# Performance work log

Measured on AMD Instinct MI355X. Metric: run time of the kernel, lower is better.

## Reference

```python
import jax, jax.numpy as jnp
import numpy as np

B, T, D = 2, 2048, 2048
H, G = 16, 4            # query heads, kv groups
HD = D // H             # head_dim = 128
GS = H // G             # group_size = 4
EPS = 1e-6
ROPE_BASE = 10000.0


def setup_inputs() -> dict:
    key = jax.random.key(0)
    ks = jax.random.split(key, 5)
    s = 0.02
    return {
        "x": jax.random.normal(ks[0], (B, T, D), jnp.float32),
        "Wq": jax.random.normal(ks[1], (H * HD, D), jnp.float32) * s,
        "Wk": jax.random.normal(ks[2], (G * HD, D), jnp.float32) * s,
        "Wv": jax.random.normal(ks[3], (G * HD, D), jnp.float32) * s,
        "Wo": jax.random.normal(ks[4], (D, H * HD), jnp.float32) * s,
        "qn_w": jnp.ones((HD,), jnp.float32),
        "kn_w": jnp.ones((HD,), jnp.float32),
    }


def _rmsnorm(x, w):
    var = jnp.mean(x * x, axis=-1, keepdims=True)
    return x * jax.lax.rsqrt(var + EPS) * w


def _rope_tables(t, d):
    inv_freq = 1.0 / (ROPE_BASE ** (jnp.arange(0, d, 2, dtype=jnp.float32) / d))
    freqs = jnp.arange(t, dtype=jnp.float32)[:, None] * inv_freq[None, :]
    emb = jnp.concatenate([freqs, freqs], axis=-1)  # [T, d]
    return jnp.cos(emb), jnp.sin(emb)


def _apply_rope(x, cos, sin):
    # x: [b, h, t, d]
    d2 = x.shape[-1] // 2
    x1, x2 = x[..., :d2], x[..., d2:]
    rot = jnp.concatenate([-x2, x1], axis=-1)
    return x * cos + rot * sin


def reference(x, Wq, Wk, Wv, Wo, qn_w, kn_w):
    b, t, _ = x.shape
    q = (x @ Wq.T).reshape(b, t, H, HD).transpose(0, 2, 1, 3)  # [b,H,t,hd]
    k = (x @ Wk.T).reshape(b, t, G, HD).transpose(0, 2, 1, 3)  # [b,G,t,hd]
    v = (x @ Wv.T).reshape(b, t, G, HD).transpose(0, 2, 1, 3)

    q = _rmsnorm(q, qn_w)
    k = _rmsnorm(k, kn_w)

    cos, sin = _rope_tables(t, HD)
    q = _apply_rope(q, cos, sin)
    k = _apply_rope(k, cos, sin)

    # torch code scales q by hd^-0.5, then SDPA applies default hd^-0.5 again
    scale = (HD ** -0.5) * (HD ** -0.5)

    # GQA without materializing repeat_interleave: group query heads
    qg = q.reshape(b, G, GS, t, HD)
    scores = jnp.einsum("bgxqd,bgkd->bgxqk", qg, k) * scale  # [b,G,GS,t,t]
    causal = jnp.tril(jnp.ones((t, t), bool))
    scores = jnp.where(causal, scores, -jnp.inf)
    attn = jax.nn.softmax(scores, axis=-1)
    ctx = jnp.einsum("bgxqk,bgkd->bgxqd", attn, v)  # [b,G,GS,t,hd]
    ctx = ctx.reshape(b, H, t, HD).transpose(0, 2, 1, 3).reshape(b, t, H * HD)
    return ctx @ Wo.T
```

## Files before the change

kernel.cpp:

```cpp
#include <hip/hip_runtime.h>
#include <hip/hip_bf16.h>

#define B_ 2
#define T_ 2048
#define D_ 2048
#define H_ 16
#define G_ 4
#define HD_ 128
#define GS_ (H_/G_)

typedef _Float16 half8 __attribute__((ext_vector_type(8)));
typedef _Float16 half2_t __attribute__((ext_vector_type(2)));
typedef float f32x4 __attribute__((ext_vector_type(4)));
typedef float f32x16 __attribute__((ext_vector_type(16)));
typedef int int4_t __attribute__((ext_vector_type(4)));

#define KV_TILE_BYTES 35840
#define KROW_F16 136
#define VROW_F16 72
#define VBASE_F16 8704

__global__ void cvt_f16(const float* __restrict__ in, _Float16* __restrict__ out, int n) {
    int i = blockIdx.x * blockDim.x + threadIdx.x;
    int stride = blockDim.x * gridDim.x;
    for (; i < n; i += stride) out[i] = (_Float16)in[i];
}

__global__ void rope_tables_k(float* __restrict__ cosT, float* __restrict__ sinT) {
    int i = blockIdx.x * blockDim.x + threadIdx.x;
    int t = i >> 6, l = i & 63;
    float inv_freq = powf(10000.0f, -((float)(2 * l)) / 128.0f);
    float a = (float)t * inv_freq;
    cosT[i] = cosf(a);
    sinT[i] = sinf(a);
}

__global__ void __launch_bounds__(256) gemm_tile(const _Float16* __restrict__ A,
                                                 const _Float16* __restrict__ B0,
                                                 float* __restrict__ C0, int n0t,
                                                 const _Float16* __restrict__ B1,
                                                 float* __restrict__ C1, int n1t,
                                                 const _Float16* __restrict__ B2,
                                                 float* __restrict__ C2, int n2t,
                                                 int Kd) {
    __shared__ _Float16 sA[128 * 32];
    __shared__ _Float16 sB[128 * 32];

    int tid = threadIdx.x;
    int w = tid >> 6, lane = tid & 63;
    int l15 = lane & 15, g4 = lane >> 4;
    int wm = w >> 1, wn = w & 1;

    int y = blockIdx.y;
    const _Float16* Bsel;
    float* Csel;
    int ldc, cb;
    if (y < n0t)            { Bsel = B0; Csel = C0; ldc = n0t * 128; cb = y; }
    else if (y < n0t + n1t) { Bsel = B1; Csel = C1; ldc = n1t * 128; cb = y - n0t; }
    else                    { Bsel = B2; Csel = C2; ldc = n2t * 128; cb = y - n0t - n1t; }

    const _Float16* Ab = A + (size_t)(blockIdx.x * 128) * Kd;
    const _Float16* Bb = Bsel + (size_t)(cb * 128) * Kd;

    int s0 = w * 128 + lane;
    int s1 = s0 + 64;
    int r0 = s0 >> 2, c0 = s0 & 3;
    int r1 = s1 >> 2, c1 = s1 & 3;
    size_t ga0 = (size_t)r0 * Kd + c0 * 8;
    size_t ga1 = (size_t)r1 * Kd + c1 * 8;
    _Float16* lds_a0 = sA + (size_t)(w * 2) * 512;
    _Float16* lds_a1 = sA + (size_t)(w * 2 + 1) * 512;
    _Float16* lds_b0 = sB + (size_t)(w * 2) * 512;
    _Float16* lds_b1 = sB + (size_t)(w * 2 + 1) * 512;

    #define STAGE(K0)                                                                     \
        do {                                                                              \
            __builtin_amdgcn_global_load_lds(                                             \
                (const __attribute__((address_space(1))) unsigned int*)(Ab + ga0 + (K0)), \
                (__attribute__((address_space(3))) unsigned int*)lds_a0, 16, 0, 0);       \
            __builtin_amdgcn_global_load_lds(                                             \
                (const __attribute__((address_space(1))) unsigned int*)(Ab + ga1 + (K0)), \
                (__attribute__((address_space(3))) unsigned int*)lds_a1, 16, 0, 0);       \
            __builtin_amdgcn_global_load_lds(                                             \
                (const __attribute__((address_space(1))) unsigned int*)(Bb + ga0 + (K0)), \
                (__attribute__((address_space(3))) unsigned int*)lds_b0, 16, 0, 0);       \
            __builtin_amdgcn_global_load_lds(                                             \
                (const __attribute__((address_space(1))) unsigned int*)(Bb + ga1 + (K0)), \
                (__attribute__((address_space(3))) unsigned int*)lds_b1, 16, 0, 0);       \
        } while (0)

    f32x4 acc[4][4];
    #pragma unroll
    for (int i = 0; i < 4; i++)
        #pragma unroll
        for (int j = 0; j < 4; j++) acc[i][j] = (f32x4){0.f, 0.f, 0.f, 0.f};

    STAGE(0);

    int nIt = Kd >> 5;
    for (int it = 0; it < nIt; ++it) {
        __syncthreads();

        half8 af[4], bf[4];
        #pragma unroll
        for (int mi = 0; mi < 4; mi++)
            af[mi] = *(const half8*)&sA[(wm * 64 + mi * 16 + l15) * 32 + g4 * 8];
        #pragma unroll
        for (int ni = 0; ni < 4; ni++)
            bf[ni] = *(const half8*)&sB[(wn * 64 + ni * 16 + l15) * 32 + g4 * 8];

        #pragma unroll
        for (int mi = 0; mi < 4; mi++)
            #pragma unroll
            for (int ni = 0; ni < 4; ni++)
                acc[mi][ni] = __builtin_amdgcn_mfma_f32_16x16x32_f16(af[mi], bf[ni], acc[mi][ni], 0, 0, 0);

        if (it + 1 < nIt) {
            __syncthreads();
            STAGE((size_t)(it + 1) * 32);
        }
    }
    #undef STAGE

    int rbase = blockIdx.x * 128 + wm * 64 + g4 * 4;
    int cbase = cb * 128 + wn * 64 + l15;
    #pragma unroll
    for (int mi = 0; mi < 4; mi++)
        #pragma unroll
        for (int r = 0; r < 4; r++) {
            float* crow = Csel + (size_t)(rbase + mi * 16 + r) * ldc + cbase;
            #pragma unroll
            for (int ni = 0; ni < 4; ni++) crow[ni * 16] = acc[mi][ni][r];
        }
}

__global__ void rmsnorm_rope_k(float* __restrict__ X, const float* __restrict__ w,
                               const float* __restrict__ cosT, const float* __restrict__ sinT,
                               int heads, float outScale, _Float16* __restrict__ outH) {
    int gw = (int)((blockIdx.x * (size_t)blockDim.x + threadIdx.x) >> 6);
    int lane = threadIdx.x & 63;
    float* row = X + (size_t)gw * HD_;
    int t = (gw / heads) % T_;
    float x0 = row[lane];
    float x1 = row[lane + 64];
    float ss = x0 * x0 + x1 * x1;
    #pragma unroll
    for (int off = 1; off < 64; off <<= 1) ss += __shfl_xor(ss, off);
    float inv = rsqrtf(ss * (1.0f / 128.0f) + 1e-6f);
    float n0 = x0 * inv * w[lane];
    float n1 = x1 * inv * w[lane + 64];
    float c = cosT[t * 64 + lane];
    float s = sinT[t * 64 + lane];
    float r0 = (n0 * c - n1 * s) * outScale;
    float r1 = (n1 * c + n0 * s) * outScale;
    if (outH) {
        outH[(size_t)gw * HD_ + lane]      = (_Float16)r0;
        outH[(size_t)gw * HD_ + lane + 64] = (_Float16)r1;
    } else {
        row[lane]      = r0;
        row[lane + 64] = r1;
    }
}

__global__ void __launch_bounds__(256) pack_kv(const float* __restrict__ kf,
                                               const float* __restrict__ vf,
                                               _Float16* __restrict__ img) {
    int bid = blockIdx.x;
    int tile = bid & 31, g = (bid >> 5) & 3, b = bid >> 7;
    int tid = threadIdx.x;
    _Float16* out = img + (size_t)bid * (KV_TILE_BYTES / 2);

    #pragma unroll
    for (int it = 0; it < 5; it++) {
        int gi = tid + 256 * it;
        if (gi < 64 * 17) {
            int key = gi / 17, gr = gi % 17;
            half8 hv = (half8){0, 0, 0, 0, 0, 0, 0, 0};
            if (gr < 16) {
                const float* src = kf + ((size_t)((b * T_ + tile * 64 + key) * G_ + g)) * HD_ + gr * 8;
                #pragma unroll
                for (int j = 0; j < 8; j++) hv[j] = (_Float16)src[j];
            }
            *(half8*)(out + (size_t)gi * 8) = hv;
        }
    }
    #pragma unroll
    for (int it = 0; it < 5; it++) {
        int vi = tid + 256 * it;
        if (vi < 128 * 9) {
            int d = vi / 9, gr = vi % 9;
            half8 hv = (half8){0, 0, 0, 0, 0, 0, 0, 0};
            if (gr < 8) {
                const float* src = vf + ((size_t)((b * T_ + tile * 64 + gr * 8) * G_ + g)) * HD_ + d;
                #pragma unroll
                for (int j = 0; j < 8; j++) hv[j] = (_Float16)src[(size_t)j * (G_ * HD_)];
            }
            *(half8*)(out + VBASE_F16 + (size_t)vi * 8) = hv;
        }
    }
}

__global__ void __launch_bounds__(256, 2) attn_mfma4(const _Float16* __restrict__ qh,
                                                     const _Float16* __restrict__ kvimg,
                                                     _Float16* __restrict__ ctx) {
    int id = blockIdx.x;
    int hlf = id >> 8, rr0 = id & 255;
    int qb = hlf ? (15 - (rr0 & 15)) : (rr0 & 15);
    int hb = (rr0 >> 4) | (hlf << 4);
    int h = hb & 15, b = hb >> 4;
    int g = h >> 2;

    int tid = threadIdx.x;
    int w = tid >> 6, lane = tid & 63;
    int l31 = lane & 31, hi = lane >> 5;

    __shared__ __align__(16) char sKV[2][KV_TILE_BYTES];

    int qW = qb * 128 + w * 32;
    int qme = qW + l31;

    half8 qfrag[8];
    {
        const _Float16* qrow = qh + ((size_t)(b * T_ + qme)) * (H_ * HD_) + h * HD_ + hi * 8;
        #pragma unroll
        for (int ks = 0; ks < 8; ks++) qfrag[ks] = *(const half8*)(qrow + ks * 16);
    }

    f32x16 o[4];
    #pragma unroll
    for (int dt2 = 0; dt2 < 4; dt2++)
        #pragma unroll
        for (int r = 0; r < 16; r++) o[dt2][r] = 0.f;
    float m = -INFINITY, lsum = 0.f;

    const char* ibase = (const char*)kvimg + (size_t)((b * 4 + g) * 32) * KV_TILE_BYTES;

    #define STAGE_T(BUF, KT)                                                                       \
        do {                                                                                       \
            const char* src_ = ibase + (size_t)(KT) * KV_TILE_BYTES;                               \
            char* dst_ = &sKV[BUF][0];                                                             \
            _Pragma("unroll")                                                                      \
            for (int i_ = 0; i_ < 9; i_++) {                                                       \
                int c_ = w + 4 * i_;                                                               \
                if (c_ < 35) {                                                                     \
                    __builtin_amdgcn_global_load_lds(                                              \
                        (const __attribute__((address_space(1))) unsigned int*)(src_ + c_ * 1024 + lane * 16), \
                        (__attribute__((address_space(3))) unsigned int*)(dst_ + c_ * 1024 + lane * 16), 16, 0, 0); \
                }                                                                                  \
            }                                                                                      \
        } while (0)

    int nt = 2 * qb + 2;
    int ktmax_w = (qW + 31) >> 6;

    STAGE_T(0, 0);
    int cur = 0;

    for (int kt = 0; kt < nt; kt++) {
        __syncthreads();
        if (kt + 1 < nt) STAGE_T(cur ^ 1, kt + 1);

        if (kt <= ktmax_w) {
            const char* bufK = &sKV[cur][0];
            const char* bufV = &sKV[cur][0] + VBASE_F16 * 2;

            f32x16 stc[2];
            #pragma unroll
            for (int kt2 = 0; kt2 < 2; kt2++)
                #pragma unroll
                for (int r = 0; r < 16; r++) stc[kt2][r] = 0.f;

            __builtin_amdgcn_s_setprio(1);
            #pragma unroll
            for (int ks = 0; ks < 8; ks++) {
                #pragma unroll
                for (int kt2 = 0; kt2 < 2; kt2++) {
                    half8 kfr = *(const half8*)(bufK + (kt2 * 32 + l31) * (KROW_F16 * 2) + ks * 32 + hi * 16);
                    stc[kt2] = __builtin_amdgcn_mfma_f32_32x32x16_f16(kfr, qfrag[ks], stc[kt2], 0, 0, 0);
                }
            }
            __builtin_amdgcn_s_setprio(0);

            #pragma unroll
            for (int kt2 = 0; kt2 < 2; kt2++)
                #pragma unroll
                for (int reg = 0; reg < 16; reg++) {
                    int key = kt * 64 + kt2 * 32 + 8 * (reg >> 2) + 4 * hi + (reg & 3);
                    float v = stc[kt2][reg];
                    stc[kt2][reg] = (key <= qme) ? v : -INFINITY;
                }

            float pmax = -INFINITY;
            #pragma unroll
            for (int kt2 = 0; kt2 < 2; kt2++)
                #pragma unroll
                for (int reg = 0; reg < 16; reg++) pmax = fmaxf(pmax, stc[kt2][reg]);
            pmax = fmaxf(pmax, __shfl_xor(pmax, 32));

            if (__any(!(pmax - m <= 8.0f))) {
                float nm = fmaxf(m, pmax);
                float alpha = __expf(m - nm);
                lsum *= alpha;
                #pragma unroll
                for (int reg = 0; reg < 16; reg++) {
                    float ar = __shfl(alpha, 8 * (reg >> 2) + 4 * hi + (reg & 3));
                    #pragma unroll
                    for (int dt2 = 0; dt2 < 4; dt2++) o[dt2][reg] *= ar;
                }
                m = nm;
            }

            float rsum = 0.f;
            #pragma unroll
            for (int kt2 = 0; kt2 < 2; kt2++)
                #pragma unroll
                for (int reg = 0; reg < 16; reg++) {
                    float e = __expf(stc[kt2][reg] - m);
                    stc[kt2][reg] = e;
                    rsum += e;
                }
            rsum += __shfl_xor(rsum, 32);
            lsum += rsum;

            int pk[16];
            #pragma unroll
            for (int kt2 = 0; kt2 < 2; kt2++)
                #pragma unroll
                for (int oo = 0; oo < 4; oo++)
                    #pragma unroll
                    for (int c = 0; c < 2; c++) {
                        half2_t hp;
                        hp[0] = (_Float16)stc[kt2][4 * oo + 2 * c];
                        hp[1] = (_Float16)stc[kt2][4 * oo + 2 * c + 1];
                        pk[kt2 * 8 + 2 * oo + c] = __builtin_bit_cast(int, hp);
                    }

            __builtin_amdgcn_s_setprio(1);
            #pragma unroll
            for (int ks = 0; ks < 4; ks++) {
                int base = (ks >> 1) * 8 + (ks & 1) * 4;
                int z0 = hi ? pk[base + 0] : pk[base + 2];
                int z1 = hi ? pk[base + 1] : pk[base + 3];
                int xz0 = __shfl_xor(z0, 32);
                int xz1 = __shfl_xor(z1, 32);
                int4_t pi;
                pi[0] = hi ? xz0 : pk[base + 0];
                pi[1] = hi ? xz1 : pk[base + 1];
                pi[2] = hi ? pk[base + 2] : xz0;
                pi[3] = hi ? pk[base + 3] : xz1;
                half8 pfrag = __builtin_bit_cast(half8, pi);
                #pragma unroll
                for (int dt2 = 0; dt2 < 4; dt2++) {
                    half8 vfr = *(const half8*)(bufV + (dt2 * 32 + l31) * (VROW_F16 * 2) + ks * 32 + hi * 16);
                    o[dt2] = __builtin_amdgcn_mfma_f32_32x32x16_f16(pfrag, vfr, o[dt2], 0, 0, 0);
                }
            }
            __builtin_amdgcn_s_setprio(0);
        }
        cur ^= 1;
    }
    #undef STAGE_T

    float invl = 1.0f / lsum;
    #pragma unroll
    for (int reg = 0; reg < 16; reg++) {
        int qrow = 8 * (reg >> 2) + 4 * hi + (reg & 3);
        float ir = __shfl(invl, qrow);
        _Float16* orow = ctx + (size_t)(b * T_ + qW + qrow) * (H_ * HD_) + h * HD_ + l31;
        #pragma unroll
        for (int dt2 = 0; dt2 < 4; dt2++)
            orow[dt2 * 32] = (_Float16)(o[dt2][reg] * ir);
    }
}

extern "C" void kernel_launch(void* const* d_in, const int* in_sizes, int n_in,
                              void* d_out, int out_size, void* d_ws, size_t ws_size,
                              hipStream_t stream) {
    const float* x   = (const float*)d_in[0];
    const float* Wq  = (const float*)d_in[1];
    const float* Wk  = (const float*)d_in[2];
    const float* Wv  = (const float*)d_in[3];
    const float* Wo  = (const float*)d_in[4];
    const float* qnw = (const float*)d_in[5];
    const float* knw = (const float*)d_in[6];
    float* out = (float*)d_out;

    char* ws = (char*)d_ws;
    size_t off = 0;
    auto alloc = [&](size_t bytes) {
        char* p = ws + off;
        off += (bytes + 255) & ~(size_t)255;
        return p;
    };
    _Float16* x_h  = (_Float16*)alloc((size_t)B_ * T_ * D_ * 2);
    _Float16* wq_h = (_Float16*)alloc((size_t)H_ * HD_ * D_ * 2);
    _Float16* wk_h = (_Float16*)alloc((size_t)G_ * HD_ * D_ * 2);
    _Float16* wv_h = (_Float16*)alloc((size_t)G_ * HD_ * D_ * 2);
    _Float16* wo_h = (_Float16*)alloc((size_t)D_ * H_ * HD_ * 2);
    float* q_f = (float*)alloc((size_t)B_ * T_ * H_ * HD_ * 4);
    float* k_f = (float*)alloc((size_t)B_ * T_ * G_ * HD_ * 4);
    float* v_f = (float*)alloc((size_t)B_ * T_ * G_ * HD_ * 4);
    _Float16* ctx_h = (_Float16*)alloc((size_t)B_ * T_ * H_ * HD_ * 2);
    float* cosT = (float*)alloc((size_t)T_ * 64 * 4);
    float* sinT = (float*)alloc((size_t)T_ * 64 * 4);

    _Float16* q_h   = x_h;
    _Float16* kvimg = wq_h;

    cvt_f16<<<2048, 256, 0, stream>>>(x,  x_h,  B_ * T_ * D_);
    cvt_f16<<<2048, 256, 0, stream>>>(Wq, wq_h, H_ * HD_ * D_);
    cvt_f16<<<1024, 256, 0, stream>>>(Wk, wk_h, G_ * HD_ * D_);
    cvt_f16<<<1024, 256, 0, stream>>>(Wv, wv_h, G_ * HD_ * D_);
    cvt_f16<<<2048, 256, 0, stream>>>(Wo, wo_h, D_ * H_ * HD_);
    rope_tables_k<<<(T_ * 64) / 256, 256, 0, stream>>>(cosT, sinT);

    gemm_tile<<<dim3(32, 24), 256, 0, stream>>>(x_h, wq_h, q_f, 16,
                                                wk_h, k_f, 4,
                                                wv_h, v_f, 4, D_);

    rmsnorm_rope_k<<<(B_ * T_ * H_) / 4, 256, 0, stream>>>(q_f, qnw, cosT, sinT, H_, 1.0f / 128.0f, q_h);
    rmsnorm_rope_k<<<(B_ * T_ * G_) / 4, 256, 0, stream>>>(k_f, knw, cosT, sinT, G_, 1.0f, nullptr);

    pack_kv<<<256, 256, 0, stream>>>(k_f, v_f, kvimg);

    attn_mfma4<<<512, 256, 0, stream>>>(q_h, kvimg, ctx_h);

    gemm_tile<<<dim3(32, 16), 256, 0, stream>>>(ctx_h, wo_h, out, 16,
                                                nullptr, nullptr, 0,
                                                nullptr, nullptr, 0, H_ * HD_);
}
```

Baseline: 248.7 us.

## Fuse conversions and norms, shrink GEMM tiles to 64x128 with block swizzle

Merges the five fp32-to-fp16 conversion launches into one vectorized kernel and merges the Q and K RMSNorm+RoPE launches into one. Switches the projection GEMMs to 64x128 tiles with a 1D grid and an XCD-style block remap, doubling the workgroup count so the CUs fill better. Per-block reuse drops (the B tile is loaded twice as often) in exchange for more parallelism and fewer launches.

```diff
diff --git a/kernel.cpp b/kernel.cpp
--- a/kernel.cpp
+++ b/kernel.cpp
@@ -20,10 +20,35 @@
 #define VROW_F16 72
 #define VBASE_F16 8704
 
-__global__ void cvt_f16(const float* __restrict__ in, _Float16* __restrict__ out, int n) {
-    int i = blockIdx.x * blockDim.x + threadIdx.x;
+#define C0_ 1048576
+#define C1_ 1572864
+#define C2_ 1703936
+#define C3_ 1835008
+#define C4_ 2359296
+__global__ void cvt_all(const float* __restrict__ sx, const float* __restrict__ sq,
+                        const float* __restrict__ sk, const float* __restrict__ sv,
+                        const float* __restrict__ so,
+                        _Float16* __restrict__ dx, _Float16* __restrict__ dq,
+                        _Float16* __restrict__ dk, _Float16* __restrict__ dv,
+                        _Float16* __restrict__ dw) {
+    int g = blockIdx.x * blockDim.x + threadIdx.x;
     int stride = blockDim.x * gridDim.x;
-    for (; i < n; i += stride) out[i] = (_Float16)in[i];
+    for (; g < C4_; g += stride) {
+        const float* src; _Float16* dst; int local;
+        if (g < C0_)      { src = sx; dst = dx; local = g; }
+        else if (g < C1_) { src = sq; dst = dq; local = g - C0_; }
+        else if (g < C2_) { src = sk; dst = dk; local = g - C1_; }
+        else if (g < C3_) { src = sv; dst = dv; local = g - C2_; }
+        else              { src = so; dst = dw; local = g - C3_; }
+        f32x4 a = *((const f32x4*)src + local * 2);
+        f32x4 b = *((const f32x4*)src + local * 2 + 1);
+        half8 hv;
+        hv[0] = (_Float16)a[0]; hv[1] = (_Float16)a[1];
+        hv[2] = (_Float16)a[2]; hv[3] = (_Float16)a[3];
+        hv[4] = (_Float16)b[0]; hv[5] = (_Float16)b[1];
+        hv[6] = (_Float16)b[2]; hv[7] = (_Float16)b[3];
+        *((half8*)dst + local) = hv;
+    }
 }
 
 __global__ void rope_tables_k(float* __restrict__ cosT, float* __restrict__ sinT) {
@@ -35,63 +60,61 @@
     sinT[i] = sinf(a);
 }
 
-__global__ void __launch_bounds__(256) gemm_tile(const _Float16* __restrict__ A,
-                                                 const _Float16* __restrict__ B0,
-                                                 float* __restrict__ C0, int n0t,
-                                                 const _Float16* __restrict__ B1,
-                                                 float* __restrict__ C1, int n1t,
-                                                 const _Float16* __restrict__ B2,
-                                                 float* __restrict__ C2, int n2t,
-                                                 int Kd) {
-    __shared__ _Float16 sA[128 * 32];
+__global__ void __launch_bounds__(256, 6) gemm_tile64(const _Float16* __restrict__ A,
+                                                      const _Float16* __restrict__ B0,
+                                                      float* __restrict__ C0, int n0t,
+                                                      const _Float16* __restrict__ B1,
+                                                      float* __restrict__ C1, int n1t,
+                                                      const _Float16* __restrict__ B2,
+                                                      float* __restrict__ C2, int n2t,
+                                                      int Kd, int nyt) {
+    __shared__ _Float16 sA[64 * 32];
     __shared__ _Float16 sB[128 * 32];
+
+    int nwg = gridDim.x;
+    int id = blockIdx.x;
+    int wg = (id & 7) * (nwg >> 3) + (id >> 3);
+    int by = wg % nyt;
+    int bx = wg / nyt;
 
     int tid = threadIdx.x;
     int w = tid >> 6, lane = tid & 63;
     int l15 = lane & 15, g4 = lane >> 4;
-    int wm = w >> 1, wn = w & 1;
-
-    int y = blockIdx.y;
+    int wm = w & 1, wn = w >> 1;
+
     const _Float16* Bsel;
     float* Csel;
     int ldc, cb;
-    if (y < n0t)            { Bsel = B0; Csel = C0; ldc = n0t * 128; cb = y; }
-    else if (y < n0t + n1t) { Bsel = B1; Csel = C1; ldc = n1t * 128; cb = y - n0t; }
-    else                    { Bsel = B2; Csel = C2; ldc = n2t * 128; cb = y - n0t - n1t; }
-
-    const _Float16* Ab = A + (size_t)(blockIdx.x * 128) * Kd;
+    if (by < n0t)            { Bsel = B0; Csel = C0; ldc = n0t * 128; cb = by; }
+    else if (by < n0t + n1t) { Bsel = B1; Csel = C1; ldc = n1t * 128; cb = by - n0t; }
+    else                     { Bsel = B2; Csel = C2; ldc = n2t * 128; cb = by - n0t - n1t; }
+
+    const _Float16* Ab = A + (size_t)(bx * 64) * Kd;
     const _Float16* Bb = Bsel + (size_t)(cb * 128) * Kd;
 
-    int s0 = w * 128 + lane;
-    int s1 = s0 + 64;
-    int r0 = s0 >> 2, c0 = s0 & 3;
-    int r1 = s1 >> 2, c1 = s1 & 3;
-    size_t ga0 = (size_t)r0 * Kd + c0 * 8;
-    size_t ga1 = (size_t)r1 * Kd + c1 * 8;
-    _Float16* lds_a0 = sA + (size_t)(w * 2) * 512;
-    _Float16* lds_a1 = sA + (size_t)(w * 2 + 1) * 512;
-    _Float16* lds_b0 = sB + (size_t)(w * 2) * 512;
-    _Float16* lds_b1 = sB + (size_t)(w * 2 + 1) * 512;
-
-    #define STAGE(K0)                                                                     \
-        do {                                                                              \
-            __builtin_amdgcn_global_load_lds(                                             \
-                (const __attribute__((address_space(1))) unsigned int*)(Ab + ga0 + (K0)), \
-                (__attribute__((address_space(3))) unsigned int*)lds_a0, 16, 0, 0);       \
-            __builtin_amdgcn_global_load_lds(                                             \
-                (const __attribute__((address_space(1))) unsigned int*)(Ab + ga1 + (K0)), \
-                (__attribute__((address_space(3))) unsigned int*)lds_a1, 16, 0, 0);       \
-            __builtin_amdgcn_global_load_lds(                                             \
-                (const __attribute__((address_space(1))) unsigned int*)(Bb + ga0 + (K0)), \
-                (__attribute__((address_space(3))) unsigned int*)lds_b0, 16, 0, 0);       \
-            __builtin_amdgcn_global_load_lds(                                             \
-                (const __attribute__((address_space(1))) unsigned int*)(Bb + ga1 + (K0)), \
-                (__attribute__((address_space(3))) unsigned int*)lds_b1, 16, 0, 0);       \
+    int sb1 = tid + 256;
+    size_t gaA  = (size_t)(tid >> 2) * Kd + (tid & 3) * 8;
+    size_t gaB1 = (size_t)(sb1 >> 2) * Kd + (sb1 & 3) * 8;
+    _Float16* dA  = sA + (size_t)tid * 8;
+    _Float16* dB0 = sB + (size_t)tid * 8;
+    _Float16* dB1 = sB + (size_t)sb1 * 8;
+
+    #define STAGE(K0)                                                                      \
+        do {                                                                               \
+            __builtin_amdgcn_global_load_lds(                                              \
+                (const __attribute__((address_space(1))) unsigned int*)(Ab + gaA + (K0)),  \
+                (__attribute__((address_space(3))) unsigned int*)dA, 16, 0, 0);            \
+            __builtin_amdgcn_global_load_lds(                                              \
+                (const __attribute__((address_space(1))) unsigned int*)(Bb + gaA + (K0)),  \
+                (__attribute__((address_space(3))) unsigned int*)dB0, 16, 0, 0);           \
+            __builtin_amdgcn_global_load_lds(                                              \
+                (const __attribute__((address_space(1))) unsigned int*)(Bb + gaB1 + (K0)), \
+                (__attribute__((address_space(3))) unsigned int*)dB1, 16, 0, 0);           \
         } while (0)
 
-    f32x4 acc[4][4];
-    #pragma unroll
-    for (int i = 0; i < 4; i++)
+    f32x4 acc[2][4];
+    #pragma unroll
+    for (int i = 0; i < 2; i++)
         #pragma unroll
         for (int j = 0; j < 4; j++) acc[i][j] = (f32x4){0.f, 0.f, 0.f, 0.f};
 
@@ -101,16 +124,16 @@
     for (int it = 0; it < nIt; ++it) {
         __syncthreads();
 
-        half8 af[4], bf[4];
-        #pragma unroll
-        for (int mi = 0; mi < 4; mi++)
-            af[mi] = *(const half8*)&sA[(wm * 64 + mi * 16 + l15) * 32 + g4 * 8];
+        half8 af[2], bf[4];
+        #pragma unroll
+        for (int mi = 0; mi < 2; mi++)
+            af[mi] = *(const half8*)&sA[(wm * 32 + mi * 16 + l15) * 32 + g4 * 8];
         #pragma unroll
         for (int ni = 0; ni < 4; ni++)
             bf[ni] = *(const half8*)&sB[(wn * 64 + ni * 16 + l15) * 32 + g4 * 8];
 
         #pragma unroll
-        for (int mi = 0; mi < 4; mi++)
+        for (int mi = 0; mi < 2; mi++)
             #pragma unroll
             for (int ni = 0; ni < 4; ni++)
                 acc[mi][ni] = __builtin_amdgcn_mfma_f32_16x16x32_f16(af[mi], bf[ni], acc[mi][ni], 0, 0, 0);
@@ -122,10 +145,10 @@
     }
     #undef STAGE
 
-    int rbase = blockIdx.x * 128 + wm * 64 + g4 * 4;
+    int rbase = bx * 64 + wm * 32 + g4 * 4;
     int cbase = cb * 128 + wn * 64 + l15;
     #pragma unroll
-    for (int mi = 0; mi < 4; mi++)
+    for (int mi = 0; mi < 2; mi++)
         #pragma unroll
         for (int r = 0; r < 4; r++) {
             float* crow = Csel + (size_t)(rbase + mi * 16 + r) * ldc + cbase;
@@ -134,28 +157,33 @@
         }
 }
 
-__global__ void rmsnorm_rope_k(float* __restrict__ X, const float* __restrict__ w,
-                               const float* __restrict__ cosT, const float* __restrict__ sinT,
-                               int heads, float outScale, _Float16* __restrict__ outH) {
+__global__ void rmsnorm_rope_qk(float* __restrict__ Qf, float* __restrict__ Kf,
+                                const float* __restrict__ qw, const float* __restrict__ kw,
+                                const float* __restrict__ cosT, const float* __restrict__ sinT,
+                                _Float16* __restrict__ qH) {
     int gw = (int)((blockIdx.x * (size_t)blockDim.x + threadIdx.x) >> 6);
     int lane = threadIdx.x & 63;
-    float* row = X + (size_t)gw * HD_;
-    int t = (gw / heads) % T_;
+    bool isQ = gw < (B_ * T_ * H_);
+    int row_i = isQ ? gw : gw - (B_ * T_ * H_);
+    int heads = isQ ? H_ : G_;
+    const float* wv = isQ ? qw : kw;
+    float* row = (isQ ? Qf : Kf) + (size_t)row_i * HD_;
+    int t = (row_i / heads) % T_;
     float x0 = row[lane];
     float x1 = row[lane + 64];
     float ss = x0 * x0 + x1 * x1;
     #pragma unroll
     for (int off = 1; off < 64; off <<= 1) ss += __shfl_xor(ss, off);
     float inv = rsqrtf(ss * (1.0f / 128.0f) + 1e-6f);
-    float n0 = x0 * inv * w[lane];
-    float n1 = x1 * inv * w[lane + 64];
+    float n0 = x0 * inv * wv[lane];
+    float n1 = x1 * inv * wv[lane + 64];
     float c = cosT[t * 64 + lane];
     float s = sinT[t * 64 + lane];
-    float r0 = (n0 * c - n1 * s) * outScale;
-    float r1 = (n1 * c + n0 * s) * outScale;
-    if (outH) {
-        outH[(size_t)gw * HD_ + lane]      = (_Float16)r0;
-        outH[(size_t)gw * HD_ + lane + 64] = (_Float16)r1;
+    float r0 = n0 * c - n1 * s;
+    float r1 = n1 * c + n0 * s;
+    if (isQ) {
+        qH[(size_t)row_i * HD_ + lane]      = (_Float16)(r0 * (1.0f / 128.0f));
+        qH[(size_t)row_i * HD_ + lane + 64] = (_Float16)(r1 * (1.0f / 128.0f));
     } else {
         row[lane]      = r0;
         row[lane + 64] = r1;
@@ -407,25 +435,20 @@
     _Float16* q_h   = x_h;
     _Float16* kvimg = wq_h;
 
-    cvt_f16<<<2048, 256, 0, stream>>>(x,  x_h,  B_ * T_ * D_);
-    cvt_f16<<<2048, 256, 0, stream>>>(Wq, wq_h, H_ * HD_ * D_);
-    cvt_f16<<<1024, 256, 0, stream>>>(Wk, wk_h, G_ * HD_ * D_);
-    cvt_f16<<<1024, 256, 0, stream>>>(Wv, wv_h, G_ * HD_ * D_);
-    cvt_f16<<<2048, 256, 0, stream>>>(Wo, wo_h, D_ * H_ * HD_);
+    cvt_all<<<2048, 256, 0, stream>>>(x, Wq, Wk, Wv, Wo, x_h, wq_h, wk_h, wv_h, wo_h);
     rope_tables_k<<<(T_ * 64) / 256, 256, 0, stream>>>(cosT, sinT);
 
-    gemm_tile<<<dim3(32, 24), 256, 0, stream>>>(x_h, wq_h, q_f, 16,
-                                                wk_h, k_f, 4,
-                                                wv_h, v_f, 4, D_);
-
-    rmsnorm_rope_k<<<(B_ * T_ * H_) / 4, 256, 0, stream>>>(q_f, qnw, cosT, sinT, H_, 1.0f / 128.0f, q_h);
-    rmsnorm_rope_k<<<(B_ * T_ * G_) / 4, 256, 0, stream>>>(k_f, knw, cosT, sinT, G_, 1.0f, nullptr);
+    gemm_tile64<<<64 * 24, 256, 0, stream>>>(x_h, wq_h, q_f, 16,
+                                             wk_h, k_f, 4,
+                                             wv_h, v_f, 4, D_, 24);
+
+    rmsnorm_rope_qk<<<(B_ * T_ * (H_ + G_)) / 4, 256, 0, stream>>>(q_f, k_f, qnw, knw, cosT, sinT, q_h);
 
     pack_kv<<<256, 256, 0, stream>>>(k_f, v_f, kvimg);
 
     attn_mfma4<<<512, 256, 0, stream>>>(q_h, kvimg, ctx_h);
 
-    gemm_tile<<<dim3(32, 16), 256, 0, stream>>>(ctx_h, wo_h, out, 16,
-                                                nullptr, nullptr, 0,
-                                                nullptr, nullptr, 0, H_ * HD_);
-}
+    gemm_tile64<<<64 * 16, 256, 0, stream>>>(ctx_h, wo_h, out, 16,
+                                             nullptr, nullptr, 0,
+                                             nullptr, nullptr, 0, H_ * HD_, 16);
+}
```

After: 253.3 us. No clear change (+1.9%).
